# Optimization experiments

Measured on AMD Instinct MI355X. Metric: run time of the kernel, lower is better.

The kernel has to match this reference:

```python
import jax, jax.numpy as jnp
import numpy as np

B, D, A, H, NH = 32768, 768, 17, 128, 4
DH = H // NH


def _ln(x, g, b, eps=1e-5):
    mu = jnp.mean(x, axis=-1, keepdims=True)
    var = jnp.mean((x - mu) ** 2, axis=-1, keepdims=True)
    return (x - mu) / jnp.sqrt(var + eps) * g + b


def setup_inputs() -> dict:
    key = jax.random.key(0)
    ks = jax.random.split(key, 16)
    s = 0.02
    return {
        "visual_feat": jax.random.normal(ks[0], (B, D), jnp.float32),
        "au_feat": jax.random.uniform(ks[1], (B, A), jnp.float32),
        "w_tok": jax.random.normal(ks[2], (H, 1), jnp.float32) * s,
        "b_tok": jnp.zeros((H,), jnp.float32),
        "pos": jax.random.normal(ks[3], (1, A, H), jnp.float32) * s,
        "g_auln": jnp.ones((H,), jnp.float32),
        "b_auln": jnp.zeros((H,), jnp.float32),
        "w_q": jax.random.normal(ks[4], (H, D), jnp.float32) * s,
        "b_q": jnp.zeros((H,), jnp.float32),
        "w_in": jax.random.normal(ks[5], (3 * H, H), jnp.float32) * s,  # packed q,k,v in_proj
        "b_in": jnp.zeros((3 * H,), jnp.float32),
        "w_ao": jax.random.normal(ks[6], (H, H), jnp.float32) * s,  # MHA out_proj
        "b_ao": jnp.zeros((H,), jnp.float32),
        "g_aln": jnp.ones((H,), jnp.float32),
        "b_aln": jnp.zeros((H,), jnp.float32),
        "w_out": jax.random.normal(ks[7], (D, H), jnp.float32) * s,
        "b_out": jnp.zeros((D,), jnp.float32),
        "w_gate": jax.random.normal(ks[8], (D, 2 * D), jnp.float32) * s,
        "b_gate": jnp.zeros((D,), jnp.float32),
    }


def reference(visual_feat, au_feat, w_tok, b_tok, pos, g_auln, b_auln,
              w_q, b_q, w_in, b_in, w_ao, b_ao, g_aln, b_aln,
              w_out, b_out, w_gate, b_gate):
    # AU tokens: Linear(1 -> H) on intensities, + pos embed, LN. [B, A, H]
    au_tokens = au_feat[..., None] * w_tok[:, 0] + b_tok
    au_tokens = _ln(au_tokens + pos, g_auln, b_auln)
    # query: [B, H] (seq len 1)
    query = visual_feat @ w_q.T + b_q
    # MultiheadAttention (batch_first, packed in_proj)
    wq, wk, wv = w_in[:H], w_in[H:2 * H], w_in[2 * H:]
    bq, bk, bv = b_in[:H], b_in[H:2 * H], b_in[2 * H:]
    q = (query @ wq.T + bq).reshape(-1, NH, DH)          # [B, nh, dh]
    k = (au_tokens @ wk.T + bk).reshape(-1, A, NH, DH)   # [B, A, nh, dh]
    v = (au_tokens @ wv.T + bv).reshape(-1, A, NH, DH)
    scale = 1.0 / jnp.sqrt(jnp.asarray(DH, q.dtype))
    scores = jnp.einsum('bhd,bahd->bha', q * scale, k)   # [B, nh, A]
    attn = jax.nn.softmax(scores, axis=-1)
    ctx = jnp.einsum('bha,bahd->bhd', attn, v).reshape(-1, H)
    attn_out = ctx @ w_ao.T + b_ao
    attn_out = _ln(attn_out, g_aln, b_aln)
    attn_feat = attn_out @ w_out.T + b_out               # [B, D]
    gate_in = jnp.concatenate([visual_feat, attn_feat], axis=1)
    gate = jax.nn.sigmoid(gate_in @ w_gate.T + b_gate)
    return gate * attn_feat + (1.0 - gate) * visual_feat
```

## Files before the change

### kernel.cpp

```cpp
#include <hip/hip_runtime.h>
#include <hip/hip_bf16.h>

typedef __hip_bfloat16 bf16;
typedef __attribute__((ext_vector_type(8))) short short8;
typedef __attribute__((ext_vector_type(4))) float f32x4;
typedef __attribute__((ext_vector_type(8))) __bf16 bf16x8;
typedef const __attribute__((address_space(1))) void* gas_ptr;
typedef __attribute__((address_space(3))) void* las_ptr;

#define NB 32768
#define DD 768
#define AA 17
#define HH 128

__device__ __forceinline__ short f2bs(float f){
  bf16 h = __float2bfloat16(f);
  return __builtin_bit_cast(short, h);
}
__device__ __forceinline__ f32x4 mfma16(short8 a, short8 b, f32x4 c){
  return __builtin_amdgcn_mfma_f32_16x16x32_bf16(
      __builtin_bit_cast(bf16x8, a), __builtin_bit_cast(bf16x8, b), c, 0, 0, 0);
}
__device__ __forceinline__ void glds16(const short* g, short* l){
  __builtin_amdgcn_global_load_lds((gas_ptr)g, (las_ptr)l, 16, 0, 0);
}

template<int F32>
__device__ __forceinline__ short8 ldchunk(const void* base, long elem_off){
  if (F32){
    const float4* p = (const float4*)((const float*)base + elem_off);
    float4 x = p[0], y = p[1];
    short8 r;
    r[0]=f2bs(x.x); r[1]=f2bs(x.y); r[2]=f2bs(x.z); r[3]=f2bs(x.w);
    r[4]=f2bs(y.x); r[5]=f2bs(y.y); r[6]=f2bs(y.z); r[7]=f2bs(y.w);
    return r;
  } else {
    return *(const short8*)((const short*)base + elem_off);
  }
}


__device__ __forceinline__ float blk_mean128(float v, float* tmp){
  int t = threadIdx.x;
  #pragma unroll
  for (int m = 32; m; m >>= 1) v += __shfl_xor(v, m);
  if ((t & 63) == 0) tmp[t >> 6] = v;
  __syncthreads();
  float r = (tmp[0] + tmp[1]) * (1.0f / 128.0f);
  __syncthreads();
  return r;
}

__global__ void prep1(const float* __restrict__ w_tok, const float* __restrict__ b_tok,
                      const float* __restrict__ pos, const float* __restrict__ g_auln,
                      float* __restrict__ ug, float* __restrict__ rg, float* __restrict__ coef){
  __shared__ float tmp[2];
  int h = threadIdx.x;
  float w = w_tok[h];
  float wbar = blk_mean128(w, tmp);
  float u = w - wbar;
  float g = g_auln[h];
  ug[h] = u * g;
  float muu = blk_mean128(u * u, tmp);
  if (h == 0) coef[0] = muu;
  float bt = b_tok[h];
  for (int a = 0; a < AA; ++a){
    float c = bt + pos[a * HH + h];
    float cbar = blk_mean128(c, tmp);
    float r = c - cbar;
    rg[a * HH + h] = r * g;
    float mur = blk_mean128(u * r, tmp);
    float mrr = blk_mean128(r * r, tmp);
    if (h == 0){ coef[1 + a] = mur; coef[18 + a] = mrr; }
  }
}

__global__ void prep2(const float* __restrict__ w_in, const float* __restrict__ b_in,
                      const float* __restrict__ b_auln, const float* __restrict__ b_q,
                      const float* __restrict__ ug, const float* __restrict__ rg,
                      float* __restrict__ Uk, float* __restrict__ Ck,
                      float* __restrict__ Uv, float* __restrict__ Cv,
                      float* __restrict__ Rk, float* __restrict__ Rv,
                      float* __restrict__ bqf){
  int hp = threadIdx.x, bid = blockIdx.x;
  const float* wqrow = w_in + (long)hp * HH;
  const float* wkrow = w_in + (long)(HH + hp) * HH;
  const float* wvrow = w_in + (long)(2 * HH + hp) * HH;
  if (bid < AA){
    int a = bid;
    float sk = 0.f, sv = 0.f;
    for (int t = 0; t < HH; ++t){
      float r = rg[a * HH + t];
      sk += r * wkrow[t];
      sv += r * wvrow[t];
    }
    Rk[a * HH + hp] = sk; Rv[a * HH + hp] = sv;
  } else if (bid == AA){
    float uk = 0.f, uv = 0.f, ck = 0.f, cv = 0.f;
    for (int t = 0; t < HH; ++t){
      float u = ug[t], ba = b_auln[t];
      float wk = wkrow[t], wv = wvrow[t];
      uk += u * wk; uv += u * wv; ck += ba * wk; cv += ba * wv;
    }
    Uk[hp] = uk; Uv[hp] = uv;
    Ck[hp] = ck + b_in[HH + hp];
    Cv[hp] = cv + b_in[2 * HH + hp];
  } else {
    float s = 0.f;
    for (int t = 0; t < HH; ++t) s += b_q[t] * wqrow[t];
    bqf[hp] = s + b_in[hp];
  }
}

__global__ void prep_wqf(const float* __restrict__ w_in, const float* __restrict__ w_q,
                         bf16* __restrict__ Wqf){
  __shared__ float wq[HH];
  int h = blockIdx.x, t = threadIdx.x;
  if (t < HH) wq[t] = w_in[(long)h * HH + t];
  __syncthreads();
  for (int j = t; j < DD; j += 256){
    float acc = 0.f;
    for (int k = 0; k < HH; ++k) acc += wq[k] * w_q[(long)k * DD + j];
    Wqf[(long)h * DD + j] = __float2bfloat16(acc);
  }
}

__global__ void prep_gate(const float* __restrict__ w_gate, const float* __restrict__ b_gate,
                          const float* __restrict__ w_out, const float* __restrict__ b_out,
                          const float* __restrict__ w_ao,
                          bf16* __restrict__ Wg1b, bf16* __restrict__ Wg2w,
                          bf16* __restrict__ Woutb, float* __restrict__ bgp,
                          bf16* __restrict__ w_ao_bf){
  __shared__ float wg2[DD];
  __shared__ float red[2];
  int c = blockIdx.x, t = threadIdx.x;
  const float* wrow = w_gate + (long)c * (2 * DD);
  for (int j = t; j < DD; j += 128){
    Wg1b[(long)c * DD + j] = __float2bfloat16(wrow[j]);
    wg2[j] = wrow[DD + j];
  }
  if (c < HH) w_ao_bf[(long)c * HH + t] = __float2bfloat16(w_ao[(long)c * HH + t]);
  __syncthreads();
  float acc = 0.f;
  for (int j = 0; j < DD; ++j) acc = fmaf(wg2[j], w_out[(long)j * HH + t], acc);
  Wg2w[(long)c * HH + t] = __float2bfloat16(acc);
  Woutb[(long)c * HH + t] = __float2bfloat16(w_out[(long)c * HH + t]);
  float pb = 0.f;
  for (int j = t; j < DD; j += 128) pb = fmaf(wg2[j], b_out[j], pb);
  #pragma unroll
  for (int m = 32; m; m >>= 1) pb += __shfl_xor(pb, m);
  if ((t & 63) == 0) red[t >> 6] = pb;
  __syncthreads();
  if (t == 0) bgp[c] = b_gate[c] + red[0] + red[1];
}

__global__ __launch_bounds__(128) void attn(
    const bf16* __restrict__ Q, const float* __restrict__ au, const float* __restrict__ coef,
    const float* __restrict__ Uk_, const float* __restrict__ Ck_,
    const float* __restrict__ Uv_, const float* __restrict__ Cv_,
    const float* __restrict__ Rk, const float* __restrict__ Rv,
    bf16* __restrict__ ctx){
  const int ROWS = 8;
  int h = threadIdx.x;
  long row0 = (long)blockIdx.x * ROWS;
  float Uk = Uk_[h], Ck = Ck_[h], Uv = Uv_[h], Cv = Cv_[h];
  float cA = coef[0];
  float rk[AA], rv[AA];
  #pragma unroll
  for (int a = 0; a < AA; ++a){
    rk[a] = Rk[a * HH + h];
    rv[a] = Rv[a * HH + h];
  }
  __shared__ float sa[ROWS * AA];
  for (int idx = h; idx < ROWS * AA; idx += 128)
    sa[idx] = au[row0 * AA + idx];
  __syncthreads();
  const float scale = 0.17677669529663689f;
  for (int r = 0; r < ROWS; ++r){
    long row = row0 + r;
    float q = __bfloat162float(Q[row * HH + h]);
    float sc[AA], vv[AA];
    #pragma unroll
    for (int a = 0; a < AA; ++a){
      float s = sa[r * AA + a];
      float var = fmaf(s * s, cA, fmaf(2.f * s, coef[1 + a], coef[18 + a]));
      float rinv = rsqrtf(fmaxf(var, 0.f) + 1e-5f);
      float kk = fmaf(s, Uk, rk[a]) * rinv + Ck;
      vv[a]    = fmaf(s, Uv, rv[a]) * rinv + Cv;
      float p = q * kk;
      p += __shfl_xor(p, 16); p += __shfl_xor(p, 8); p += __shfl_xor(p, 4);
      p += __shfl_xor(p, 2);  p += __shfl_xor(p, 1);
      sc[a] = p * scale;
    }
    float mx = sc[0];
    #pragma unroll
    for (int a = 1; a < AA; ++a) mx = fmaxf(mx, sc[a]);
    float den = 0.f, cval = 0.f;
    #pragma unroll
    for (int a = 0; a < AA; ++a){
      float e = __expf(sc[a] - mx);
      den += e; cval += e * vv[a];
    }
    ctx[row * HH + h] = __float2bfloat16(cval / den);
  }
}

template<int MODE, int AF, int SIDE>
__global__ __launch_bounds__(128) void gemm_n128(
    const void* __restrict__ A, long lda, int ks,
    const bf16* __restrict__ Bw, long ldb,
    const float* __restrict__ bias,
    const float* __restrict__ g_ln, const float* __restrict__ b_ln,
    short* __restrict__ sideA,
    bf16* __restrict__ C)
{
  __shared__ __align__(16) short smem[10240];
  const int tid = threadIdx.x;
  const int wv = tid >> 6, l = tid & 63;
  const long rowBase = (long)blockIdx.x * 32;
  const int fr = l & 15, kq = l >> 4;
  const int swofs = (kq ^ ((l >> 1) & 3)) << 3;
  const int arow = tid >> 2, ac = tid & 3;
  const int asl = (ac ^ ((arow >> 1) & 3)) * 8;
  const int srow = l >> 2;
  const int schunk = ((l & 3) ^ ((l >> 3) & 3)) * 8;

  f32x4 acc[8];
  f32x4 zero = {0.f, 0.f, 0.f, 0.f};
  #pragma unroll
  for (int j = 0; j < 8; ++j) acc[j] = zero;

  short8 avh;
  {
    short8 av0 = ldchunk<AF>(A, (rowBase + arow) * lda + ac * 8);
    if (SIDE) *(short8*)(sideA + (rowBase + arow) * lda + ac * 8) = av0;
    *(short8*)(smem + arow * 32 + asl) = av0;
    #pragma unroll
    for (int i = 0; i < 4; ++i){
      const int brow = wv * 64 + i * 16 + srow;
      glds16((const short*)Bw + (long)brow * ldb + schunk,
             smem + 1024 + wv * 2048 + i * 512);
    }
    if (ks > 1){
      avh = ldchunk<AF>(A, (rowBase + arow) * lda + 32 + ac * 8);
      if (SIDE) *(short8*)(sideA + (rowBase + arow) * lda + 32 + ac * 8) = avh;
    }
  }
  for (int kt = 0; kt < ks; ++kt){
    __syncthreads();
    short* cb = smem + (kt & 1) * 5120;
    short* nb = smem + ((kt + 1) & 1) * 5120;
    if (kt + 1 < ks){
      *(short8*)(nb + arow * 32 + asl) = avh;
      const long kB = (long)(kt + 1) * 32;
      #pragma unroll
      for (int i = 0; i < 4; ++i){
        const int brow = wv * 64 + i * 16 + srow;
        glds16((const short*)Bw + (long)brow * ldb + kB + schunk,
               nb + 1024 + wv * 2048 + i * 512);
      }
      if (kt + 2 < ks){
        const long kA = (long)(kt + 2) * 32;
        avh = ldchunk<AF>(A, (rowBase + arow) * lda + kA + ac * 8);
        if (SIDE) *(short8*)(sideA + (rowBase + arow) * lda + kA + ac * 8) = avh;
      }
    }
    const int ra = wv * 16 + fr;
    short8 a0 = *(const short8*)(cb + ra * 32 + swofs);
    #pragma unroll
    for (int nt = 0; nt < 8; ++nt){
      short8 b = *(const short8*)(cb + 1024 + (nt * 16 + fr) * 32 + swofs);
      acc[nt] = mfma16(a0, b, acc[nt]);
    }
  }
  __syncthreads();

  short* ep = smem;
  if (MODE == 1){
    #pragma unroll
    for (int r = 0; r < 4; ++r){
      float x[8]; float sm = 0.f, sq = 0.f;
      #pragma unroll
      for (int nt = 0; nt < 8; ++nt){
        x[nt] = acc[nt][r] + bias[nt * 16 + fr];
        sm += x[nt]; sq += x[nt] * x[nt];
      }
      sm += __shfl_xor(sm, 1); sq += __shfl_xor(sq, 1);
      sm += __shfl_xor(sm, 2); sq += __shfl_xor(sq, 2);
      sm += __shfl_xor(sm, 4); sq += __shfl_xor(sq, 4);
      sm += __shfl_xor(sm, 8); sq += __shfl_xor(sq, 8);
      const float mu = sm * (1.f / 128.f);
      const float var = sq * (1.f / 128.f) - mu * mu;
      const float rinv = rsqrtf(fmaxf(var, 0.f) + 1e-5f);
      const int lrow = wv * 16 + kq * 4 + r;
      #pragma unroll
      for (int nt = 0; nt < 8; ++nt){
        const int col = nt * 16 + fr;
        float y = (x[nt] - mu) * rinv * g_ln[col] + b_ln[col];
        ep[lrow * 136 + col] = f2bs(y);
      }
    }
  } else {
    #pragma unroll
    for (int nt = 0; nt < 8; ++nt){
      const float bv = bias[nt * 16 + fr];
      #pragma unroll
      for (int r = 0; r < 4; ++r)
        ep[(wv * 16 + kq * 4 + r) * 136 + nt * 16 + fr] = f2bs(acc[nt][r] + bv);
    }
  }
  __syncthreads();

  #pragma unroll
  for (int it = 0; it < 4; ++it){
    const int cid = tid + it * 128;
    const int rw = cid >> 4;
    const int cc = (cid & 15) * 8;
    *(short8*)((short*)C + (rowBase + rw) * HH + cc) = *(const short8*)(ep + rw * 136 + cc);
  }
}

template<int A1F>
__global__ __launch_bounds__(256) void gemm_final(
    const void* __restrict__ A1,
    const bf16* __restrict__ aon,
    const bf16* __restrict__ Wg1b,
    const bf16* __restrict__ Wg2w,
    const bf16* __restrict__ Woutb,
    const float* __restrict__ bgp,
    const float* __restrict__ b_out,
    const float* __restrict__ vf,
    float* __restrict__ C)
{
  __shared__ __align__(16) short smem[12288];
  const int tid = threadIdx.x;
  const int wv = tid >> 6, l = tid & 63;

  const int nx = 12;
  const int bid = blockIdx.y * nx + blockIdx.x;
  const int cpx = (NB / 128) * nx / 8;
  const int swz = (bid & 7) * cpx + (bid >> 3);
  const long rowBase = (long)(swz / nx) * 128;
  const int colBase = (swz % nx) * 64;

  const int fr = l & 15;
  const int kq = l >> 4;
  const int swofs = (kq ^ ((l >> 1) & 3)) << 3;
  const int srow = l >> 2;
  const int schunk = ((l & 3) ^ ((l >> 3) & 3)) * 8;

  f32x4 accG[2][4], accF[2][4];
  f32x4 zero = {0.f, 0.f, 0.f, 0.f};
  #pragma unroll
  for (int i = 0; i < 2; ++i)
    #pragma unroll
    for (int j = 0; j < 4; ++j){ accG[i][j] = zero; accF[i][j] = zero; }

  if (A1F == 0){
    const short* Ab = (const short*)A1;
    const short* Bb = (const short*)Wg1b;
    #define STAGE_F1(p, kt) {                                                 \
      short* d = smem + (p) * 6144;                                           \
      _Pragma("unroll")                                                       \
      for (int i = 0; i < 2; ++i){                                            \
        const int r = wv * 32 + i * 16 + srow;                                \
        glds16(Ab + (rowBase + r) * (long)DD + (kt) * 32 + schunk,            \
               d + wv * 1024 + i * 512);                                      \
      }                                                                       \
      glds16(Bb + (long)(colBase + wv * 16 + srow) * DD + (kt) * 32 + schunk, \
             d + 4096 + wv * 512);                                            \
    }
    STAGE_F1(0, 0);
    for (int kt = 0; kt < DD / 32; ++kt){
      __syncthreads();
      if (kt + 1 < DD / 32) STAGE_F1((kt + 1) & 1, kt + 1);
      short* cb = smem + (kt & 1) * 6144;
      const int ra0 = wv * 32 + fr;
      short8 a0 = *(const short8*)(cb + ra0 * 32 + swofs);
      short8 a1 = *(const short8*)(cb + (ra0 + 16) * 32 + swofs);
      #pragma unroll
      for (int nt = 0; nt < 4; ++nt){
        short8 b = *(const short8*)(cb + 4096 + (nt * 16 + fr) * 32 + swofs);
        accG[0][nt] = mfma16(a0, b, accG[0][nt]);
        accG[1][nt] = mfma16(a1, b, accG[1][nt]);
      }
    }
    #undef STAGE_F1
  } else {
    const int r0 = tid >> 2, ac = tid & 3;
    const int s0 = (ac ^ ((r0 >> 1) & 3)) * 8;
    for (int kt = 0; kt < DD / 32; ++kt){
      const long kA = (long)kt * 32;
      short8 av0 = ldchunk<1>(A1, (rowBase + r0) * (long)DD + kA + ac * 8);
      short8 av1 = ldchunk<1>(A1, (rowBase + 64 + r0) * (long)DD + kA + ac * 8);
      short8 bv  = *(const short8*)((const short*)Wg1b + (long)(colBase + r0) * DD + kA + ac * 8);
      __syncthreads();
      *(short8*)(smem + r0 * 32 + s0) = av0;
      *(short8*)(smem + (64 + r0) * 32 + s0) = av1;
      *(short8*)(smem + 4096 + r0 * 32 + s0) = bv;
      __syncthreads();
      const int ra0 = wv * 32 + fr;
      short8 a0 = *(const short8*)(smem + ra0 * 32 + swofs);
      short8 a1 = *(const short8*)(smem + (ra0 + 16) * 32 + swofs);
      #pragma unroll
      for (int nt = 0; nt < 4; ++nt){
        short8 b = *(const short8*)(smem + 4096 + (nt * 16 + fr) * 32 + swofs);
        accG[0][nt] = mfma16(a0, b, accG[0][nt]);
        accG[1][nt] = mfma16(a1, b, accG[1][nt]);
      }
    }
  }

  for (int kt = 0; kt < HH / 32; ++kt){
    __syncthreads();
    const long kA = (long)kt * 32;
    #pragma unroll
    for (int i = 0; i < 2; ++i){
      const int r = wv * 32 + i * 16 + srow;
      glds16((const short*)aon + (rowBase + r) * HH + kA + schunk,
             smem + wv * 1024 + i * 512);
    }
    glds16((const short*)Wg2w + (long)(colBase + wv * 16 + srow) * HH + kA + schunk,
           smem + 4096 + wv * 512);
    glds16((const short*)Woutb + (long)(colBase + wv * 16 + srow) * HH + kA + schunk,
           smem + 6144 + wv * 512);
    __syncthreads();
    const int ra0 = wv * 32 + fr;
    short8 a0 = *(const short8*)(smem + ra0 * 32 + swofs);
    short8 a1 = *(const short8*)(smem + (ra0 + 16) * 32 + swofs);
    #pragma unroll
    for (int nt = 0; nt < 4; ++nt){
      short8 b  = *(const short8*)(smem + 4096 + (nt * 16 + fr) * 32 + swofs);
      short8 b2 = *(const short8*)(smem + 6144 + (nt * 16 + fr) * 32 + swofs);
      accG[0][nt] = mfma16(a0, b,  accG[0][nt]);
      accG[1][nt] = mfma16(a1, b,  accG[1][nt]);
      accF[0][nt] = mfma16(a0, b2, accF[0][nt]);
      accF[1][nt] = mfma16(a1, b2, accF[1][nt]);
    }
  }

  float bg[4], bo[4];
  #pragma unroll
  for (int nt = 0; nt < 4; ++nt){
    const int col = colBase + nt * 16 + fr;
    bg[nt] = bgp[col];
    bo[nt] = b_out[col];
  }
  #pragma unroll
  for (int mt = 0; mt < 2; ++mt){
    const long r0 = rowBase + wv * 32 + mt * 16 + kq * 4;
    #pragma unroll
    for (int r = 0; r < 4; ++r){
      const long row = r0 + r;
      const float* vrow = vf + row * DD;
      float* crow = C + row * DD;
      #pragma unroll
      for (int nt = 0; nt < 4; ++nt){
        const int col = colBase + nt * 16 + fr;
        const float lin = accG[mt][nt][r] + bg[nt];
        const float afv = accF[mt][nt][r] + bo[nt];
        const float gate = 1.f / (1.f + __expf(-lin));
        crow[col] = gate * afv + (1.f - gate) * vrow[col];
      }
    }
  }
}

extern "C" void kernel_launch(void* const* d_in, const int* in_sizes, int n_in,
                              void* d_out, int out_size, void* d_ws, size_t ws_size,
                              hipStream_t stream){
  const float* visual = (const float*)d_in[0];
  const float* au     = (const float*)d_in[1];
  const float* w_tok  = (const float*)d_in[2];
  const float* b_tok  = (const float*)d_in[3];
  const float* pos    = (const float*)d_in[4];
  const float* g_auln = (const float*)d_in[5];
  const float* b_auln = (const float*)d_in[6];
  const float* w_q    = (const float*)d_in[7];
  const float* b_q    = (const float*)d_in[8];
  const float* w_in   = (const float*)d_in[9];
  const float* b_in   = (const float*)d_in[10];
  const float* w_ao   = (const float*)d_in[11];
  const float* b_ao   = (const float*)d_in[12];
  const float* g_aln  = (const float*)d_in[13];
  const float* b_aln  = (const float*)d_in[14];
  const float* w_out  = (const float*)d_in[15];
  const float* b_out  = (const float*)d_in[16];
  const float* w_gate = (const float*)d_in[17];
  const float* b_gate = (const float*)d_in[18];

  char* ob = (char*)d_out;
  bf16* Q   = (bf16*)(ob);
  bf16* ctx = (bf16*)(ob + ((size_t)8 << 20));
  char* p = ob + ((size_t)16 << 20);
  auto alloc = [&](size_t bytes){ char* r = p; p += (bytes + 255) & ~(size_t)255; return r; };
  bf16*  Wqf     = (bf16*) alloc((size_t)HH * DD * 2);
  bf16*  w_ao_bf = (bf16*) alloc((size_t)HH * HH * 2);
  float* bqf  = (float*)alloc(HH * 4);
  float* ug   = (float*)alloc(HH * 4);
  float* rg   = (float*)alloc(AA * HH * 4);
  float* coef = (float*)alloc(64 * 4);
  float* Uk   = (float*)alloc(HH * 4);
  float* Ck   = (float*)alloc(HH * 4);
  float* Uv   = (float*)alloc(HH * 4);
  float* Cv   = (float*)alloc(HH * 4);
  float* Rk   = (float*)alloc(AA * HH * 4);
  float* Rv   = (float*)alloc(AA * HH * 4);

  char* q = (char*)d_ws;
  auto walloc = [&](size_t bytes){ char* r = q; q += (bytes + 255) & ~(size_t)255; return r; };
  bf16*  aon   = (bf16*) walloc((size_t)NB * HH * 2);
  bf16*  Wg1b  = (bf16*) walloc((size_t)DD * DD * 2);
  bf16*  Wg2w  = (bf16*) walloc((size_t)DD * HH * 2);
  bf16*  Woutb = (bf16*) walloc((size_t)DD * HH * 2);
  float* bgp   = (float*)walloc(DD * 4);
  bf16*  vbf   = (bf16*) walloc((size_t)NB * DD * 2);
  const bool use_vbf = (size_t)(q - (char*)d_ws) <= ws_size;

  prep1<<<dim3(1), dim3(128), 0, stream>>>(w_tok, b_tok, pos, g_auln, ug, rg, coef);
  prep2<<<dim3(19), dim3(128), 0, stream>>>(w_in, b_in, b_auln, b_q, ug, rg, Uk, Ck, Uv, Cv, Rk, Rv, bqf);
  prep_wqf<<<dim3(128), dim3(256), 0, stream>>>(w_in, w_q, Wqf);
  prep_gate<<<dim3(DD), dim3(128), 0, stream>>>(w_gate, b_gate, w_out, b_out, w_ao,
                                                Wg1b, Wg2w, Woutb, bgp, w_ao_bf);

  if (use_vbf)
    gemm_n128<0, 1, 1><<<dim3(NB / 32), dim3(128), 0, stream>>>(
        visual, (long)DD, DD / 32, Wqf, (long)DD,
        bqf, nullptr, nullptr, (short*)vbf, Q);
  else
    gemm_n128<0, 1, 0><<<dim3(NB / 32), dim3(128), 0, stream>>>(
        visual, (long)DD, DD / 32, Wqf, (long)DD,
        bqf, nullptr, nullptr, nullptr, Q);

  attn<<<dim3(NB / 8), dim3(128), 0, stream>>>(Q, au, coef, Uk, Ck, Uv, Cv, Rk, Rv, ctx);

  gemm_n128<1, 0, 0><<<dim3(NB / 32), dim3(128), 0, stream>>>(
      ctx, (long)HH, HH / 32, w_ao_bf, (long)HH,
      b_ao, g_aln, b_aln, nullptr, aon);

  if (use_vbf)
    gemm_final<0><<<dim3(12, NB / 128), dim3(256), 0, stream>>>(
        vbf, aon, Wg1b, Wg2w, Woutb, bgp, b_out, visual, (float*)d_out);
  else
    gemm_final<1><<<dim3(12, NB / 128), dim3(256), 0, stream>>>(
        visual, aon, Wg1b, Wg2w, Woutb, bgp, b_out, visual, (float*)d_out);
}
```

Measured before the change: 483.8 us.

## Fuse query GEMM, attention and out-proj LayerNorm into one kernel; triple-buffer final GEMM

Merges the Q projection GEMM, the per-row AU attention and the out_proj GEMM with LayerNorm into a single kernel that keeps the Q and ctx tiles in shared memory. This drops the global round trips for Q and ctx and two kernel launches. Separately, the final gate GEMM moves from double to triple buffering, waiting with explicit vmcnt instead of a full sync so loads run further ahead. Both changes use more LDS per block, which may lower occupancy, and the serial 32-row attention loop in a 128-thread block may limit parallelism.

```diff
diff --git a/kernel.cpp b/kernel.cpp
--- a/kernel.cpp
+++ b/kernel.cpp
@@ -13,6 +13,10 @@
 #define AA 17
 #define HH 128
 
+__device__ __forceinline__ float bs2f(short s){
+  unsigned int u = ((unsigned int)(unsigned short)s) << 16;
+  return __builtin_bit_cast(float, u);
+}
 __device__ __forceinline__ short f2bs(float f){
   bf16 h = __float2bfloat16(f);
   return __builtin_bit_cast(short, h);
@@ -154,67 +158,20 @@
   if (t == 0) bgp[c] = b_gate[c] + red[0] + red[1];
 }
 
-__global__ __launch_bounds__(128) void attn(
-    const bf16* __restrict__ Q, const float* __restrict__ au, const float* __restrict__ coef,
+template<int SIDE>
+__global__ __launch_bounds__(128) void qaon(
+    const float* __restrict__ visual, const bf16* __restrict__ Wqf,
+    const float* __restrict__ bqf,
+    const float* __restrict__ au, const float* __restrict__ coef,
     const float* __restrict__ Uk_, const float* __restrict__ Ck_,
     const float* __restrict__ Uv_, const float* __restrict__ Cv_,
     const float* __restrict__ Rk, const float* __restrict__ Rv,
-    bf16* __restrict__ ctx){
-  const int ROWS = 8;
-  int h = threadIdx.x;
-  long row0 = (long)blockIdx.x * ROWS;
-  float Uk = Uk_[h], Ck = Ck_[h], Uv = Uv_[h], Cv = Cv_[h];
-  float cA = coef[0];
-  float rk[AA], rv[AA];
-  #pragma unroll
-  for (int a = 0; a < AA; ++a){
-    rk[a] = Rk[a * HH + h];
-    rv[a] = Rv[a * HH + h];
-  }
-  __shared__ float sa[ROWS * AA];
-  for (int idx = h; idx < ROWS * AA; idx += 128)
-    sa[idx] = au[row0 * AA + idx];
-  __syncthreads();
-  const float scale = 0.17677669529663689f;
-  for (int r = 0; r < ROWS; ++r){
-    long row = row0 + r;
-    float q = __bfloat162float(Q[row * HH + h]);
-    float sc[AA], vv[AA];
-    #pragma unroll
-    for (int a = 0; a < AA; ++a){
-      float s = sa[r * AA + a];
-      float var = fmaf(s * s, cA, fmaf(2.f * s, coef[1 + a], coef[18 + a]));
-      float rinv = rsqrtf(fmaxf(var, 0.f) + 1e-5f);
-      float kk = fmaf(s, Uk, rk[a]) * rinv + Ck;
-      vv[a]    = fmaf(s, Uv, rv[a]) * rinv + Cv;
-      float p = q * kk;
-      p += __shfl_xor(p, 16); p += __shfl_xor(p, 8); p += __shfl_xor(p, 4);
-      p += __shfl_xor(p, 2);  p += __shfl_xor(p, 1);
-      sc[a] = p * scale;
-    }
-    float mx = sc[0];
-    #pragma unroll
-    for (int a = 1; a < AA; ++a) mx = fmaxf(mx, sc[a]);
-    float den = 0.f, cval = 0.f;
-    #pragma unroll
-    for (int a = 0; a < AA; ++a){
-      float e = __expf(sc[a] - mx);
-      den += e; cval += e * vv[a];
-    }
-    ctx[row * HH + h] = __float2bfloat16(cval / den);
-  }
-}
-
-template<int MODE, int AF, int SIDE>
-__global__ __launch_bounds__(128) void gemm_n128(
-    const void* __restrict__ A, long lda, int ks,
-    const bf16* __restrict__ Bw, long ldb,
-    const float* __restrict__ bias,
-    const float* __restrict__ g_ln, const float* __restrict__ b_ln,
+    const bf16* __restrict__ w_ao_bf, const float* __restrict__ b_ao,
+    const float* __restrict__ g_aln, const float* __restrict__ b_aln,
     short* __restrict__ sideA,
-    bf16* __restrict__ C)
+    bf16* __restrict__ aon)
 {
-  __shared__ __align__(16) short smem[10240];
+  __shared__ __align__(16) short smem[16384];
   const int tid = threadIdx.x;
   const int wv = tid >> 6, l = tid & 63;
   const long rowBase = (long)blockIdx.x * 32;
@@ -225,6 +182,9 @@
   const int srow = l >> 2;
   const int schunk = ((l & 3) ^ ((l >> 3) & 3)) * 8;
 
+  float* auS = (float*)(smem + 10240);
+  for (int idx = tid; idx < 32 * AA; idx += 128) auS[idx] = au[rowBase * AA + idx];
+
   f32x4 acc[8];
   f32x4 zero = {0.f, 0.f, 0.f, 0.f};
   #pragma unroll
@@ -232,37 +192,35 @@
 
   short8 avh;
   {
-    short8 av0 = ldchunk<AF>(A, (rowBase + arow) * lda + ac * 8);
-    if (SIDE) *(short8*)(sideA + (rowBase + arow) * lda + ac * 8) = av0;
+    short8 av0 = ldchunk<1>(visual, (rowBase + arow) * (long)DD + ac * 8);
+    if (SIDE) *(short8*)(sideA + (rowBase + arow) * DD + ac * 8) = av0;
     *(short8*)(smem + arow * 32 + asl) = av0;
     #pragma unroll
     for (int i = 0; i < 4; ++i){
       const int brow = wv * 64 + i * 16 + srow;
-      glds16((const short*)Bw + (long)brow * ldb + schunk,
+      glds16((const short*)Wqf + (long)brow * DD + schunk,
              smem + 1024 + wv * 2048 + i * 512);
     }
-    if (ks > 1){
-      avh = ldchunk<AF>(A, (rowBase + arow) * lda + 32 + ac * 8);
-      if (SIDE) *(short8*)(sideA + (rowBase + arow) * lda + 32 + ac * 8) = avh;
-    }
-  }
-  for (int kt = 0; kt < ks; ++kt){
+    avh = ldchunk<1>(visual, (rowBase + arow) * (long)DD + 32 + ac * 8);
+    if (SIDE) *(short8*)(sideA + (rowBase + arow) * DD + 32 + ac * 8) = avh;
+  }
+  for (int kt = 0; kt < DD / 32; ++kt){
     __syncthreads();
     short* cb = smem + (kt & 1) * 5120;
     short* nb = smem + ((kt + 1) & 1) * 5120;
-    if (kt + 1 < ks){
+    if (kt + 1 < DD / 32){
       *(short8*)(nb + arow * 32 + asl) = avh;
       const long kB = (long)(kt + 1) * 32;
       #pragma unroll
       for (int i = 0; i < 4; ++i){
         const int brow = wv * 64 + i * 16 + srow;
-        glds16((const short*)Bw + (long)brow * ldb + kB + schunk,
+        glds16((const short*)Wqf + (long)brow * DD + kB + schunk,
                nb + 1024 + wv * 2048 + i * 512);
       }
-      if (kt + 2 < ks){
+      if (kt + 2 < DD / 32){
         const long kA = (long)(kt + 2) * 32;
-        avh = ldchunk<AF>(A, (rowBase + arow) * lda + kA + ac * 8);
-        if (SIDE) *(short8*)(sideA + (rowBase + arow) * lda + kA + ac * 8) = avh;
+        avh = ldchunk<1>(visual, (rowBase + arow) * (long)DD + kA + ac * 8);
+        if (SIDE) *(short8*)(sideA + (rowBase + arow) * DD + kA + ac * 8) = avh;
       }
     }
     const int ra = wv * 16 + fr;
@@ -275,48 +233,113 @@
   }
   __syncthreads();
 
-  short* ep = smem;
-  if (MODE == 1){
-    #pragma unroll
-    for (int r = 0; r < 4; ++r){
-      float x[8]; float sm = 0.f, sq = 0.f;
+  short* ep = smem + 11328;
+  #pragma unroll
+  for (int nt = 0; nt < 8; ++nt){
+    const float bv = bqf[nt * 16 + fr];
+    #pragma unroll
+    for (int r = 0; r < 4; ++r)
+      ep[(wv * 16 + kq * 4 + r) * 136 + nt * 16 + fr] = f2bs(acc[nt][r] + bv);
+  }
+  __syncthreads();
+
+  {
+    const int h = tid;
+    const float Uk = Uk_[h], Ck = Ck_[h], Uv = Uv_[h], Cv = Cv_[h];
+    const float cA = coef[0];
+    float rk[AA], rv[AA];
+    #pragma unroll
+    for (int a = 0; a < AA; ++a){ rk[a] = Rk[a * HH + h]; rv[a] = Rv[a * HH + h]; }
+    const float scale = 0.17677669529663689f;
+    for (int r = 0; r < 32; ++r){
+      float q = bs2f(ep[r * 136 + h]);
+      float sc[AA], vvv[AA];
+      #pragma unroll
+      for (int a = 0; a < AA; ++a){
+        float s = auS[r * AA + a];
+        float var = fmaf(s * s, cA, fmaf(2.f * s, coef[1 + a], coef[18 + a]));
+        float rinv = rsqrtf(fmaxf(var, 0.f) + 1e-5f);
+        float kk = fmaf(s, Uk, rk[a]) * rinv + Ck;
+        vvv[a]   = fmaf(s, Uv, rv[a]) * rinv + Cv;
+        float p = q * kk;
+        p += __shfl_xor(p, 16); p += __shfl_xor(p, 8); p += __shfl_xor(p, 4);
+        p += __shfl_xor(p, 2);  p += __shfl_xor(p, 1);
+        sc[a] = p * scale;
+      }
+      float mx = sc[0];
+      #pragma unroll
+      for (int a = 1; a < AA; ++a) mx = fmaxf(mx, sc[a]);
+      float den = 0.f, cval = 0.f;
+      #pragma unroll
+      for (int a = 0; a < AA; ++a){
+        float e = __expf(sc[a] - mx);
+        den += e; cval += e * vvv[a];
+      }
+      ep[r * 136 + h] = f2bs(cval / den);
+    }
+  }
+  __syncthreads();
+
+  f32x4 acc2[8];
+  #pragma unroll
+  for (int j = 0; j < 8; ++j) acc2[j] = zero;
+  for (int kh = 0; kh < 2; ++kh){
+    __syncthreads();
+    #pragma unroll
+    for (int c = 0; c < 2; ++c){
+      const int kc = (kh * 2 + c) * 32;
+      #pragma unroll
+      for (int i = 0; i < 4; ++i){
+        const int row = wv * 64 + i * 16 + srow;
+        glds16((const short*)w_ao_bf + (long)row * HH + kc + schunk,
+               smem + c * 4096 + wv * 2048 + i * 512);
+      }
+    }
+    __syncthreads();
+    #pragma unroll
+    for (int c = 0; c < 2; ++c){
+      const int kt = kh * 2 + c;
+      short8 a0 = *(const short8*)(ep + (wv * 16 + fr) * 136 + kt * 32 + kq * 8);
       #pragma unroll
       for (int nt = 0; nt < 8; ++nt){
-        x[nt] = acc[nt][r] + bias[nt * 16 + fr];
-        sm += x[nt]; sq += x[nt] * x[nt];
-      }
-      sm += __shfl_xor(sm, 1); sq += __shfl_xor(sq, 1);
-      sm += __shfl_xor(sm, 2); sq += __shfl_xor(sq, 2);
-      sm += __shfl_xor(sm, 4); sq += __shfl_xor(sq, 4);
-      sm += __shfl_xor(sm, 8); sq += __shfl_xor(sq, 8);
-      const float mu = sm * (1.f / 128.f);
-      const float var = sq * (1.f / 128.f) - mu * mu;
-      const float rinv = rsqrtf(fmaxf(var, 0.f) + 1e-5f);
-      const int lrow = wv * 16 + kq * 4 + r;
-      #pragma unroll
-      for (int nt = 0; nt < 8; ++nt){
-        const int col = nt * 16 + fr;
-        float y = (x[nt] - mu) * rinv * g_ln[col] + b_ln[col];
-        ep[lrow * 136 + col] = f2bs(y);
-      }
-    }
-  } else {
+        short8 b = *(const short8*)(smem + c * 4096 + (nt * 16 + fr) * 32 + swofs);
+        acc2[nt] = mfma16(a0, b, acc2[nt]);
+      }
+    }
+  }
+  __syncthreads();
+
+  short* ep2 = smem;
+  #pragma unroll
+  for (int r = 0; r < 4; ++r){
+    float x[8]; float sm = 0.f, sq = 0.f;
     #pragma unroll
     for (int nt = 0; nt < 8; ++nt){
-      const float bv = bias[nt * 16 + fr];
-      #pragma unroll
-      for (int r = 0; r < 4; ++r)
-        ep[(wv * 16 + kq * 4 + r) * 136 + nt * 16 + fr] = f2bs(acc[nt][r] + bv);
-    }
-  }
-  __syncthreads();
-
+      x[nt] = acc2[nt][r] + b_ao[nt * 16 + fr];
+      sm += x[nt]; sq += x[nt] * x[nt];
+    }
+    sm += __shfl_xor(sm, 1); sq += __shfl_xor(sq, 1);
+    sm += __shfl_xor(sm, 2); sq += __shfl_xor(sq, 2);
+    sm += __shfl_xor(sm, 4); sq += __shfl_xor(sq, 4);
+    sm += __shfl_xor(sm, 8); sq += __shfl_xor(sq, 8);
+    const float mu = sm * (1.f / 128.f);
+    const float var = sq * (1.f / 128.f) - mu * mu;
+    const float rinv = rsqrtf(fmaxf(var, 0.f) + 1e-5f);
+    const int lrow = wv * 16 + kq * 4 + r;
+    #pragma unroll
+    for (int nt = 0; nt < 8; ++nt){
+      const int col = nt * 16 + fr;
+      float y = (x[nt] - mu) * rinv * g_aln[col] + b_aln[col];
+      ep2[lrow * 136 + col] = f2bs(y);
+    }
+  }
+  __syncthreads();
   #pragma unroll
   for (int it = 0; it < 4; ++it){
     const int cid = tid + it * 128;
     const int rw = cid >> 4;
     const int cc = (cid & 15) * 8;
-    *(short8*)((short*)C + (rowBase + rw) * HH + cc) = *(const short8*)(ep + rw * 136 + cc);
+    *(short8*)((short*)aon + (rowBase + rw) * HH + cc) = *(const short8*)(ep2 + rw * 136 + cc);
   }
 }
 
@@ -332,7 +355,7 @@
     const float* __restrict__ vf,
     float* __restrict__ C)
 {
-  __shared__ __align__(16) short smem[12288];
+  __shared__ __align__(16) short smem[18432];
   const int tid = threadIdx.x;
   const int wv = tid >> 6, l = tid & 63;
 
@@ -371,10 +394,13 @@
              d + 4096 + wv * 512);                                            \
     }
     STAGE_F1(0, 0);
+    STAGE_F1(1, 1);
     for (int kt = 0; kt < DD / 32; ++kt){
-      __syncthreads();
-      if (kt + 1 < DD / 32) STAGE_F1((kt + 1) & 1, kt + 1);
-      short* cb = smem + (kt & 1) * 6144;
+      if (kt < DD / 32 - 1) asm volatile("s_waitcnt vmcnt(3)" ::: "memory");
+      else                  asm volatile("s_waitcnt vmcnt(0)" ::: "memory");
+      __builtin_amdgcn_s_barrier();
+      if (kt + 2 < DD / 32) STAGE_F1((kt + 2) % 3, kt + 2);
+      short* cb = smem + (kt % 3) * 6144;
       const int ra0 = wv * 32 + fr;
       short8 a0 = *(const short8*)(cb + ra0 * 32 + swofs);
       short8 a1 = *(const short8*)(cb + (ra0 + 16) * 32 + swofs);
@@ -490,8 +516,6 @@
   const float* b_gate = (const float*)d_in[18];
 
   char* ob = (char*)d_out;
-  bf16* Q   = (bf16*)(ob);
-  bf16* ctx = (bf16*)(ob + ((size_t)8 << 20));
   char* p = ob + ((size_t)16 << 20);
   auto alloc = [&](size_t bytes){ char* r = p; p += (bytes + 255) & ~(size_t)255; return r; };
   bf16*  Wqf     = (bf16*) alloc((size_t)HH * DD * 2);
@@ -524,19 +548,13 @@
                                                 Wg1b, Wg2w, Woutb, bgp, w_ao_bf);
 
   if (use_vbf)
-    gemm_n128<0, 1, 1><<<dim3(NB / 32), dim3(128), 0, stream>>>(
-        visual, (long)DD, DD / 32, Wqf, (long)DD,
-        bqf, nullptr, nullptr, (short*)vbf, Q);
+    qaon<1><<<dim3(NB / 32), dim3(128), 0, stream>>>(
+        visual, Wqf, bqf, au, coef, Uk, Ck, Uv, Cv, Rk, Rv,
+        w_ao_bf, b_ao, g_aln, b_aln, (short*)vbf, aon);
   else
-    gemm_n128<0, 1, 0><<<dim3(NB / 32), dim3(128), 0, stream>>>(
-        visual, (long)DD, DD / 32, Wqf, (long)DD,
-        bqf, nullptr, nullptr, nullptr, Q);
-
-  attn<<<dim3(NB / 8), dim3(128), 0, stream>>>(Q, au, coef, Uk, Ck, Uv, Cv, Rk, Rv, ctx);
-
-  gemm_n128<1, 0, 0><<<dim3(NB / 32), dim3(128), 0, stream>>>(
-      ctx, (long)HH, HH / 32, w_ao_bf, (long)HH,
-      b_ao, g_aln, b_aln, nullptr, aon);
+    qaon<0><<<dim3(NB / 32), dim3(128), 0, stream>>>(
+        visual, Wqf, bqf, au, coef, Uk, Ck, Uv, Cv, Rk, Rv,
+        w_ao_bf, b_ao, g_aln, b_aln, nullptr, aon);
 
   if (use_vbf)
     gemm_final<0><<<dim3(12, NB / 128), dim3(256), 0, stream>>>(
```

New measurement: 490.1 us. About the same (+1.3%).
